# Optimization experiments

Hardware: AMD Instinct MI355X
Metric: run time of the kernel (lower is better)

## Reference

```python
import jax, jax.numpy as jnp
import numpy as np

N = 100000   # num visited nodes
D = 128      # emb_dim
B = 1024     # num queries (eg_idx groups)
DEG = 256    # edges per query group (fixed, > K so topk always prunes)
E = B * DEG  # 262144 edges
K = 20       # max_attended_edges
RATIO = 0.0  # ratio_update
NEG_SLOPE = 0.01  # LeakyReLU default


def segment_softmax(logits, seg, num_segments):
    m = jax.ops.segment_max(logits, seg, num_segments=num_segments)
    ex = jnp.exp(logits - m[seg])
    s = jax.ops.segment_sum(ex, seg, num_segments=num_segments)
    return ex / s[seg]


def setup_inputs() -> dict:
    key = jax.random.key(0)
    ks = jax.random.split(key, 11)
    node_score = jax.random.uniform(ks[0], (N,), dtype=jnp.float32)
    node_repr = jax.random.normal(ks[1], (N, D), dtype=jnp.float32)
    rel_emb = jax.random.normal(ks[2], (E, D), dtype=jnp.float32)
    q_src_emb = jax.random.normal(ks[3], (B, D), dtype=jnp.float32)
    q_rel_emb = jax.random.normal(ks[4], (B, D), dtype=jnp.float32)
    # G3: Linear(4D, 4D, bias=False), init normal std sqrt(2/dim_in)
    Wq = jax.random.normal(ks[5], (4 * D, 4 * D), dtype=jnp.float32) * np.sqrt(2.0 / (4 * D))
    Wk = jax.random.normal(ks[6], (4 * D, 4 * D), dtype=jnp.float32) * np.sqrt(2.0 / (4 * D))
    # linear_between_steps: Linear(D, D) xavier
    W_lin = jax.random.normal(ks[7], (D, D), dtype=jnp.float32) * np.sqrt(2.0 / (2 * D))
    b_lin = jnp.zeros((D,), dtype=jnp.float32)
    # edges: [E, 8]; col0 = eg_idx (sorted, fixed DEG per group), col6 = vi, col7 = vj
    eg = jnp.repeat(jnp.arange(B, dtype=jnp.int32), DEG)
    vi = jax.random.randint(ks[8], (E,), 0, N, dtype=jnp.int32)
    vj = jax.random.randint(ks[9], (E,), 0, N, dtype=jnp.int32)
    z = jnp.zeros((E,), dtype=jnp.int32)
    edges = jnp.stack([eg, z, z, z, z, z, vi, vj], axis=1)
    return {
        "node_score": node_score, "node_repr": node_repr, "rel_emb": rel_emb,
        "q_src_emb": q_src_emb, "q_rel_emb": q_rel_emb,
        "Wq": Wq, "Wk": Wk, "W_lin": W_lin, "b_lin": b_lin, "edges": edges,
    }


def reference(node_score, node_repr, rel_emb, q_src_emb, q_rel_emb, Wq, Wk, W_lin, b_lin, edges):
    eg = edges[:, 0]
    vi = edges[:, 6]
    vj = edges[:, 7]
    # --- G3 attention score over edges ---
    hvi = node_repr[vi]           # [E, D]
    hvj = node_repr[vj]           # [E, D]
    qst = q_src_emb[eg]           # [E, D]
    qr = q_rel_emb[eg]            # [E, D]
    left = jnp.concatenate([hvi, rel_emb, qst, qr], axis=-1)   # [E, 4D]
    right = jnp.concatenate([hvj, rel_emb, qst, qr], axis=-1)  # [E, 4D]
    logits = jnp.sum((left @ Wq.T) * (right @ Wk.T), axis=-1)  # [E]
    # --- segment softmax over source node vi ---
    sm = segment_softmax(logits, vi, N)
    src_score = node_score[vi]
    target_score = sm * src_score
    # --- per-query-group top-k edge pruning (fixed DEG per group) ---
    topk_vals, topk_idx = jax.lax.top_k(target_score.reshape(B, DEG), K)  # [B, K]
    flat_idx = (topk_idx + jnp.arange(B, dtype=topk_idx.dtype)[:, None] * DEG).reshape(-1)  # [B*K]
    p_vi = vi[flat_idx]
    p_vj = vj[flat_idx]
    p_sm = sm[flat_idx]
    p_src = src_score[flat_idx]
    # --- node score aggregation: scatter-sum sm*src_score into target node vj ---
    updated_node_score = jax.ops.segment_sum(p_sm * p_src, p_vj, num_segments=N)
    # --- node representation update (sparse transition + identity fill) ---
    agg = jax.ops.segment_sum((1.0 - RATIO) * p_sm[:, None] * node_repr[p_vj], p_vi, num_segments=N)
    appears = jnp.zeros((N,), dtype=jnp.float32).at[p_vi].set(1.0)
    self_coef = jnp.where(appears > 0, RATIO, 1.0)[:, None]
    updated_repr = agg + self_coef * node_repr
    # --- bypass_forward: LeakyReLU(Linear) ---
    updated_repr = jax.nn.leaky_relu(updated_repr @ W_lin.T + b_lin, NEG_SLOPE)
    return updated_node_score, updated_repr
```

## Files before the change

### kernel.cpp

```cpp
#include <hip/hip_runtime.h>

#define NN 100000
#define BQ 1024
#define EE 262144
#define KTOP 20

typedef unsigned long long ull;
typedef __attribute__((ext_vector_type(8))) short bf16x8;
typedef __attribute__((ext_vector_type(4))) float f32x4;

__device__ __forceinline__ ull enc64(double d) {
  ull u = (ull)__double_as_longlong(d);
  return (u >> 63) ? ~u : (u | 0x8000000000000000ull);
}
__device__ __forceinline__ double dec64(ull u) {
  ull b = (u >> 63) ? (u & 0x7FFFFFFFFFFFFFFFull) : ~u;
  return __longlong_as_double((long long)b);
}

__device__ __forceinline__ unsigned short f2bf(float f) {
  unsigned u = __float_as_uint(f);
  u += 0x7fff + ((u >> 16) & 1);
  return (unsigned short)(u >> 16);
}
__device__ __forceinline__ float bf2f(unsigned short h) {
  return __uint_as_float(((unsigned)h) << 16);
}
__device__ __forceinline__ void cvt8(float4 x, float4 y, bf16x8& hi, bf16x8& lo) {
  float a[8] = {x.x, x.y, x.z, x.w, y.x, y.y, y.z, y.w};
#pragma unroll
  for (int j = 0; j < 8; j++) {
    unsigned short h = f2bf(a[j]);
    float r = a[j] - bf2f(h);
    hi[j] = (short)h;
    lo[j] = (short)f2bf(r);
  }
}

__global__ void k_prep(const int* __restrict__ edges, int4* __restrict__ evi,
                       int* __restrict__ vi32, ull* __restrict__ menc,
                       double* __restrict__ s, float* __restrict__ appears,
                       float* __restrict__ out_score) {
  int i = blockIdx.x * 256 + threadIdx.x;
  int st = gridDim.x * 256;
  for (int e = i; e < EE; e += st) {
    int vi = edges[(size_t)e * 8 + 6];
    evi[e] = make_int4(edges[(size_t)e * 8 + 0], vi, edges[(size_t)e * 8 + 7], 0);
    vi32[e] = vi;
  }
  for (int n = i; n < NN; n += st) {
    menc[n] = 0ull;
    s[n] = 0.0;
    appears[n] = 0.f;
    out_score[n] = 0.f;
  }
}

__global__ void k_matM(const float* __restrict__ Wq, const float* __restrict__ Wk,
                       float* __restrict__ M, float* __restrict__ MT) {
  int x = blockIdx.x;
  int y = blockIdx.y * 256 + threadIdx.x;
  float acc = 0.f;
  for (int a = 0; a < 512; a++)
    acc += Wq[a * 512 + x] * Wk[a * 512 + y];
  M[x * 512 + y] = acc;
  MT[y * 512 + x] = acc;
}

__global__ void k_pack(const float* __restrict__ M, const float* __restrict__ MT,
                       const float* __restrict__ Wl,
                       short* __restrict__ wn_hi, short* __restrict__ wn_lo,
                       short* __restrict__ m11_hi, short* __restrict__ m11_lo,
                       short* __restrict__ wl_hi, short* __restrict__ wl_lo) {
  int idx = blockIdx.x * 256 + threadIdx.x;
  if (idx >= 5 * 16384) return;
  int arr = idx >> 14;
  int j16 = idx & 16383;
  int g = j16 >> 9;
  int l = (j16 >> 3) & 63;
  int jj = j16 & 7;
  int c = (g >> 2) * 16 + (l & 15);
  int k = (g & 3) * 32 + ((l >> 4) << 3) + jj;
  float v;
  short *dh, *dl;
  if (arr == 0)      { v = MT[(size_t)c * 512 + k];               dh = wn_hi;          dl = wn_lo; }
  else if (arr == 1) { v = MT[(size_t)(128 + c) * 512 + k];       dh = wn_hi + 16384;  dl = wn_lo + 16384; }
  else if (arr == 2) { v = M[(size_t)(128 + c) * 512 + k];        dh = wn_hi + 32768;  dl = wn_lo + 32768; }
  else if (arr == 3) { v = MT[(size_t)(128 + c) * 512 + 128 + k]; dh = m11_hi;         dl = m11_lo; }
  else               { v = Wl[(size_t)c * 128 + k];               dh = wl_hi;          dl = wl_lo; }
  unsigned short h = f2bf(v);
  float r = v - bf2f(h);
  dh[j16] = (short)h;
  dl[j16] = (short)f2bf(r);
}

__global__ void k_pq(const float* __restrict__ M, const float* __restrict__ MT,
                     const float* __restrict__ qsA, const float* __restrict__ qrA,
                     float* __restrict__ Qv, double* __restrict__ cq) {
  int b = blockIdx.x, d = threadIdx.x;
  __shared__ float qs[128], qr[128];
  qs[d] = qsA[b * 128 + d];
  qr[d] = qrA[b * 128 + d];
  __syncthreads();
  float uh = 0, ui = 0, ur = 0;
  for (int x = 0; x < 128; x++) {
    float qsx = qs[x], qrx = qr[x];
    uh += qsx * M[(256 + x) * 512 + d]        + qrx * M[(384 + x) * 512 + d];
    ur += qsx * M[(256 + x) * 512 + 128 + d]  + qrx * M[(384 + x) * 512 + 128 + d];
    ui += qsx * MT[(256 + x) * 512 + d]       + qrx * MT[(384 + x) * 512 + d];
    ur += qsx * MT[(256 + x) * 512 + 128 + d] + qrx * MT[(384 + x) * 512 + 128 + d];
  }
  Qv[b * 384 + d]       = uh;
  Qv[b * 384 + 128 + d] = ui;
  Qv[b * 384 + 256 + d] = ur;
  float t1 = 0, t2 = 0;
  for (int y = 0; y < 128; y++) {
    float qsy = qs[y], qry = qr[y];
    t1 += qsy * MT[(256 + y) * 512 + 256 + d] + qry * MT[(384 + y) * 512 + 256 + d];
    t2 += qsy * MT[(256 + y) * 512 + 384 + d] + qry * MT[(384 + y) * 512 + 384 + d];
  }
  float cp = qs[d] * t1 + qr[d] * t2;
  for (int off = 32; off; off >>= 1) cp += __shfl_down(cp, off, 64);
  __shared__ float red[2];
  if ((d & 63) == 0) red[d >> 6] = cp;
  __syncthreads();
  if (d == 0) cq[b] = (double)(red[0] + red[1]);
}

__global__ __launch_bounds__(512) void k_gemm_node(const float* __restrict__ A,
                                                   const short* __restrict__ WT_hi,
                                                   const short* __restrict__ WT_lo,
                                                   float* __restrict__ G,
                                                   float* __restrict__ H1,
                                                   float* __restrict__ J) {
  __shared__ __align__(16) float As[64][132];
  __shared__ __align__(16) short Bh[16384];
  float* Of = (float*)Bh;
  int t = threadIdx.x;
  int row0 = blockIdx.x * 64;
  int w = t >> 6, l = t & 63;
  int rt = w & 3;
  int c0 = (w >> 2) * 4;
#pragma unroll
  for (int i = 0; i < 4; i++) {
    int fi = t + i * 512;
    int r = fi >> 5, c4 = (fi & 31) * 4;
    float4 v = make_float4(0.f, 0.f, 0.f, 0.f);
    if (row0 + r < NN) v = *(const float4*)(A + (size_t)(row0 + r) * 128 + c4);
    *(float4*)&As[r][c4] = v;
    *(bf16x8*)&Bh[fi * 8] = *(const bf16x8*)(WT_hi + fi * 8);
  }
  __syncthreads();
  int rloc = rt * 16 + (l & 15);
  int kq = (l >> 4) * 8;
  for (int panel = 0; panel < 3; panel++) {
    const short* sl = WT_lo + panel * 16384;
    bf16x8 blv[4][4];
#pragma unroll
    for (int cc = 0; cc < 4; cc++)
#pragma unroll
      for (int kt = 0; kt < 4; kt++)
        blv[cc][kt] = *(const bf16x8*)(sl + (((c0 + cc) * 4 + kt) * 64 + l) * 8);
    f32x4 acc[4];
#pragma unroll
    for (int cc = 0; cc < 4; cc++)
#pragma unroll
      for (int j = 0; j < 4; j++) acc[cc][j] = 0.f;
#pragma unroll
    for (int kt = 0; kt < 4; kt++) {
      int kb = kt * 32 + kq;
      float4 x = *(const float4*)&As[rloc][kb];
      float4 y = *(const float4*)&As[rloc][kb + 4];
      bf16x8 ah, al;
      cvt8(x, y, ah, al);
#pragma unroll
      for (int cc = 0; cc < 4; cc++) {
        int off = (((cc + c0) * 4 + kt) * 64 + l) * 8;
        bf16x8 bhv = *(const bf16x8*)&Bh[off];
        acc[cc] = __builtin_amdgcn_mfma_f32_16x16x32_bf16(ah, bhv, acc[cc], 0, 0, 0);
        acc[cc] = __builtin_amdgcn_mfma_f32_16x16x32_bf16(al, bhv, acc[cc], 0, 0, 0);
        acc[cc] = __builtin_amdgcn_mfma_f32_16x16x32_bf16(ah, blv[cc][kt], acc[cc], 0, 0, 0);
      }
    }
    __syncthreads();
#pragma unroll
    for (int cc = 0; cc < 4; cc++) {
      int col = (c0 + cc) * 16 + (l & 15);
#pragma unroll
      for (int reg = 0; reg < 4; reg++)
        Of[(rt * 16 + (l >> 4) * 4 + reg) * 128 + col] = acc[cc][reg];
    }
    __syncthreads();
    float* dst = (panel == 0) ? G : (panel == 1) ? H1 : J;
#pragma unroll
    for (int i = 0; i < 4; i++) {
      int fi = t + i * 512;
      int r = fi >> 5, c4 = (fi & 31) * 4;
      int rr = row0 + r;
      if (rr < NN) *(float4*)&dst[(size_t)rr * 128 + c4] = *(float4*)&Of[r * 128 + c4];
    }
    if (panel < 2) {
      __syncthreads();
      const short* sh = WT_hi + (panel + 1) * 16384;
#pragma unroll
      for (int i = 0; i < 4; i++) {
        int fi = t + i * 512;
        *(bf16x8*)&Bh[fi * 8] = *(const bf16x8*)(sh + fi * 8);
      }
      __syncthreads();
    }
  }
}

__global__ __launch_bounds__(512, 1) void k_edge(const float* __restrict__ rel,
                                                 const short* __restrict__ M11T_hi,
                                                 const short* __restrict__ M11T_lo,
                                                 const int4* __restrict__ evi,
                                                 const float* __restrict__ H1,
                                                 const float* __restrict__ J,
                                                 const float* __restrict__ Qv,
                                                 float* __restrict__ rq) {
  __shared__ __align__(16) float Rs[64][132];
  __shared__ __align__(16) short Bh[16384];
  __shared__ float part[4][64];
  __shared__ float dg[64];
  __shared__ float urs[128];
  int t = threadIdx.x;
  int e0 = blockIdx.x * 64;
  int eg = e0 >> 8;
  int w = t >> 6, l = t & 63;
  int cq2 = w & 3;
  int rh = w >> 2;
  int gg = t >> 4, ll = t & 15, d = ll * 8;
  int4 edA = evi[e0 + gg * 2];
  int4 edB = evi[e0 + gg * 2 + 1];
  const float* pA1 = H1 + (size_t)edA.y * 128 + d;
  const float* pA2 = J + (size_t)edA.z * 128 + d;
  const float* pB1 = H1 + (size_t)edB.y * 128 + d;
  const float* pB2 = J + (size_t)edB.z * 128 + d;
  float4 Aa0 = *(const float4*)pA1, Aa1 = *(const float4*)(pA1 + 4);
  float4 Ab0 = *(const float4*)pA2, Ab1 = *(const float4*)(pA2 + 4);
  float4 Ba0 = *(const float4*)pB1, Ba1 = *(const float4*)(pB1 + 4);
  float4 Bb0 = *(const float4*)pB2, Bb1 = *(const float4*)(pB2 + 4);
  bf16x8 blv[2][4];
#pragma unroll
  for (int cc = 0; cc < 2; cc++)
#pragma unroll
    for (int kt = 0; kt < 4; kt++)
      blv[cc][kt] = *(const bf16x8*)(M11T_lo + (((cq2 * 2 + cc) * 4 + kt) * 64 + l) * 8);
#pragma unroll
  for (int i = 0; i < 4; i++) {
    int fi = t + i * 512;
    int r = fi >> 5, c4 = (fi & 31) * 4;
    *(float4*)&Rs[r][c4] = *(const float4*)(rel + (size_t)(e0 + r) * 128 + c4);
    *(bf16x8*)&Bh[fi * 8] = *(const bf16x8*)(M11T_hi + fi * 8);
  }
  if (t < 128) urs[t] = Qv[(size_t)eg * 384 + 256 + t];
  __syncthreads();
  int kq = (l >> 4) * 8;
  int rq4 = (l >> 4) * 4;
#pragma unroll
  for (int rt2 = 0; rt2 < 2; rt2++) {
    int rt = rh * 2 + rt2;
    int rloc = rt * 16 + (l & 15);
    f32x4 acc[2];
#pragma unroll
    for (int cc = 0; cc < 2; cc++)
#pragma unroll
      for (int j = 0; j < 4; j++) acc[cc][j] = 0.f;
#pragma unroll
    for (int kt = 0; kt < 4; kt++) {
      int kb = kt * 32 + kq;
      float4 x = *(const float4*)&Rs[rloc][kb];
      float4 y = *(const float4*)&Rs[rloc][kb + 4];
      bf16x8 ah, al;
      cvt8(x, y, ah, al);
#pragma unroll
      for (int cc = 0; cc < 2; cc++) {
        bf16x8 bhv = *(const bf16x8*)&Bh[(((cq2 * 2 + cc) * 4 + kt) * 64 + l) * 8];
        acc[cc] = __builtin_amdgcn_mfma_f32_16x16x32_bf16(ah, bhv, acc[cc], 0, 0, 0);
        acc[cc] = __builtin_amdgcn_mfma_f32_16x16x32_bf16(al, bhv, acc[cc], 0, 0, 0);
        acc[cc] = __builtin_amdgcn_mfma_f32_16x16x32_bf16(ah, blv[cc][kt], acc[cc], 0, 0, 0);
      }
    }
    float p[4] = {0.f, 0.f, 0.f, 0.f};
#pragma unroll
    for (int cc = 0; cc < 2; cc++) {
      int c = (cq2 * 2 + cc) * 16 + (l & 15);
#pragma unroll
      for (int reg = 0; reg < 4; reg++)
        p[reg] += acc[cc][reg] * Rs[rt * 16 + rq4 + reg][c];
    }
#pragma unroll
    for (int reg = 0; reg < 4; reg++) {
      p[reg] += __shfl_xor(p[reg], 1, 64);
      p[reg] += __shfl_xor(p[reg], 2, 64);
      p[reg] += __shfl_xor(p[reg], 4, 64);
      p[reg] += __shfl_xor(p[reg], 8, 64);
    }
    if ((l & 15) == 0) {
#pragma unroll
      for (int reg = 0; reg < 4; reg++) part[cq2][rt * 16 + rq4 + reg] = p[reg];
    }
  }
  float4 u0 = *(const float4*)&urs[d], u1 = *(const float4*)&urs[d + 4];
  {
    int le = gg * 2;
    float4 r0 = *(const float4*)&Rs[le][d], r1 = *(const float4*)&Rs[le][d + 4];
    float dot = (Aa0.x + Ab0.x + u0.x) * r0.x + (Aa0.y + Ab0.y + u0.y) * r0.y
              + (Aa0.z + Ab0.z + u0.z) * r0.z + (Aa0.w + Ab0.w + u0.w) * r0.w
              + (Aa1.x + Ab1.x + u1.x) * r1.x + (Aa1.y + Ab1.y + u1.y) * r1.y
              + (Aa1.z + Ab1.z + u1.z) * r1.z + (Aa1.w + Ab1.w + u1.w) * r1.w;
    dot += __shfl_xor(dot, 1, 64);
    dot += __shfl_xor(dot, 2, 64);
    dot += __shfl_xor(dot, 4, 64);
    dot += __shfl_xor(dot, 8, 64);
    if (ll == 0) dg[le] = dot;
  }
  {
    int le = gg * 2 + 1;
    float4 r0 = *(const float4*)&Rs[le][d], r1 = *(const float4*)&Rs[le][d + 4];
    float dot = (Ba0.x + Bb0.x + u0.x) * r0.x + (Ba0.y + Bb0.y + u0.y) * r0.y
              + (Ba0.z + Bb0.z + u0.z) * r0.z + (Ba0.w + Bb0.w + u0.w) * r0.w
              + (Ba1.x + Bb1.x + u1.x) * r1.x + (Ba1.y + Bb1.y + u1.y) * r1.y
              + (Ba1.z + Bb1.z + u1.z) * r1.z + (Ba1.w + Bb1.w + u1.w) * r1.w;
    dot += __shfl_xor(dot, 1, 64);
    dot += __shfl_xor(dot, 2, 64);
    dot += __shfl_xor(dot, 4, 64);
    dot += __shfl_xor(dot, 8, 64);
    if (ll == 0) dg[le] = dot;
  }
  __syncthreads();
  if (t < 64)
    rq[e0 + t] = ((part[0][t] + part[1][t]) + (part[2][t] + part[3][t])) + dg[t];
}

__global__ __launch_bounds__(256) void k_logits(const int4* __restrict__ evi,
                                                const float* __restrict__ nrep,
                                                const float* __restrict__ G,
                                                const float* __restrict__ Qv,
                                                const double* __restrict__ cq,
                                                const float* __restrict__ rq,
                                                double* __restrict__ logits,
                                                ull* __restrict__ menc) {
  int t = threadIdx.x;
  int ll = t & 15;
  int grp = (t & 63) >> 4;
  int wid = blockIdx.x * 4 + (t >> 6);
  int nw = gridDim.x * 4;
  int d = ll * 8;
  for (int e4 = wid; e4 < EE / 4; e4 += nw) {
    int e = e4 * 4 + grp;
    int4 ed = evi[e];
    int eg = ed.x, vi = ed.y, vj = ed.z;
    const float* gp = G + (size_t)vi * 128 + d;
    const float* hi = nrep + (size_t)vi * 128 + d;
    const float* hj = nrep + (size_t)vj * 128 + d;
    const float* q  = Qv + (size_t)eg * 384 + d;
    float4 g0  = *(const float4*)gp,        g1  = *(const float4*)(gp + 4);
    float4 a0  = *(const float4*)hi,        a1  = *(const float4*)(hi + 4);
    float4 b0  = *(const float4*)hj,        b1  = *(const float4*)(hj + 4);
    float4 uh0 = *(const float4*)q,         uh1 = *(const float4*)(q + 4);
    float4 ui0 = *(const float4*)(q + 128), ui1 = *(const float4*)(q + 132);
    float acc;
    acc  = (g0.x + uh0.x) * b0.x + (g0.y + uh0.y) * b0.y
         + (g0.z + uh0.z) * b0.z + (g0.w + uh0.w) * b0.w
         + (g1.x + uh1.x) * b1.x + (g1.y + uh1.y) * b1.y
         + (g1.z + uh1.z) * b1.z + (g1.w + uh1.w) * b1.w;
    acc += ui0.x * a0.x + ui0.y * a0.y + ui0.z * a0.z + ui0.w * a0.w
         + ui1.x * a1.x + ui1.y * a1.y + ui1.z * a1.z + ui1.w * a1.w;
    acc += __shfl_xor(acc, 1, 64);
    acc += __shfl_xor(acc, 2, 64);
    acc += __shfl_xor(acc, 4, 64);
    acc += __shfl_xor(acc, 8, 64);
    if (ll == 0) {
      double l2 = (double)acc + cq[eg] + (double)rq[e];
      logits[e] = l2;
      atomicMax(&menc[vi], enc64(l2));
    }
  }
}

__global__ void k_exp(const int* __restrict__ vi32, const ull* __restrict__ menc,
                      const double* __restrict__ logits, double* __restrict__ ex,
                      double* __restrict__ s, float4* __restrict__ agg) {
  int i = blockIdx.x * 256 + threadIdx.x;
  int st = gridDim.x * 256;
  for (int e = i; e < EE; e += st) {
    int vi = vi32[e];
    double m = dec64(menc[vi]);
    double v = exp(logits[e] - m);
    ex[e] = v;
    atomicAdd(&s[vi], v);
  }
  const int n4 = NN * 32;
  for (int n = i; n < n4; n += st) agg[n] = make_float4(0.f, 0.f, 0.f, 0.f);
}

__global__ void k_topk(const double* __restrict__ ex, const double* __restrict__ s,
                       const float* __restrict__ nscore, const int4* __restrict__ evi,
                       const float* __restrict__ nrep, float* __restrict__ out_score,
                       float* __restrict__ agg, float* __restrict__ appears) {
  int b = blockIdx.x, t = threadIdx.x;
  int e = b * 256 + t;
  int vi_t = evi[e].y;
  double v = ex[e] / s[vi_t] * (double)nscore[vi_t];
  __shared__ double cv[80];
  __shared__ int ci[80];
  __shared__ int winners[KTOP];
  int w = t >> 6;
  for (int k = 0; k < KTOP; k++) {
    double bv = v;
    int bi = t;
    for (int off = 32; off; off >>= 1) {
      double ov = __shfl_down(bv, off, 64);
      int oi = __shfl_down(bi, off, 64);
      if (ov > bv || (ov == bv && oi < bi)) { bv = ov; bi = oi; }
    }
    bi = __shfl(bi, 0, 64);
    if ((t & 63) == 0) { cv[w * KTOP + k] = bv; ci[w * KTOP + k] = bi; }
    if (t == bi) v = -1.0;
  }
  __syncthreads();
  if (t < 64) {
    double v0 = cv[t];
    int i0 = ci[t];
    double v1 = (t < 16) ? cv[64 + t] : -2.0;
    int i1 = (t < 16) ? ci[64 + t] : (1 << 30);
    for (int k = 0; k < KTOP; k++) {
      double bv; int bi;
      if (v1 > v0 || (v1 == v0 && i1 < i0)) { bv = v1; bi = i1; }
      else                                  { bv = v0; bi = i0; }
      for (int off = 32; off; off >>= 1) {
        double ov = __shfl_down(bv, off, 64);
        int oi = __shfl_down(bi, off, 64);
        if (ov > bv || (ov == bv && oi < bi)) { bv = ov; bi = oi; }
      }
      bi = __shfl(bi, 0, 64);
      if (t == 0) winners[k] = bi;
      if (i0 == bi) v0 = -2.0;
      if (i1 == bi) v1 = -2.0;
    }
  }
  __syncthreads();
  for (int k = 0; k < KTOP; k++) {
    int we = b * 256 + winners[k];
    int4 ew = evi[we];
    int vi = ew.y, vj = ew.z;
    double sm = ex[we] / s[vi];
    if (t < 128) {
      atomicAdd(&agg[(size_t)vi * 128 + t], (float)sm * nrep[(size_t)vj * 128 + t]);
    } else if (t == 128) {
      atomicAdd(&out_score[vj], (float)(sm * (double)nscore[vi]));
    } else if (t == 129) {
      appears[vi] = 1.f;
    }
  }
}

__global__ __launch_bounds__(512) void k_final(const float* __restrict__ agg,
                                               const float* __restrict__ appears,
                                               const float* __restrict__ nrep,
                                               const short* __restrict__ Wl_hi,
                                               const short* __restrict__ Wl_lo,
                                               const float* __restrict__ bl,
                                               float* __restrict__ outr) {
  __shared__ __align__(16) float Xs[64][132];
  __shared__ __align__(16) short Bh[16384];
  int t = threadIdx.x;
  int row0 = blockIdx.x * 64;
  int w = t >> 6, l = t & 63;
  int rt = w & 3;
  int c0 = (w >> 2) * 4;
  bf16x8 blv[4][4];
#pragma unroll
  for (int cc = 0; cc < 4; cc++)
#pragma unroll
    for (int kt = 0; kt < 4; kt++)
      blv[cc][kt] = *(const bf16x8*)(Wl_lo + (((c0 + cc) * 4 + kt) * 64 + l) * 8);
#pragma unroll
  for (int i = 0; i < 4; i++) {
    int fi = t + i * 512;
    int r = fi >> 5, c4 = (fi & 31) * 4;
    int rr = row0 + r;
    float4 v = make_float4(0.f, 0.f, 0.f, 0.f);
    if (rr < NN) {
      float4 ag = *(const float4*)(agg + (size_t)rr * 128 + c4);
      float4 h = *(const float4*)(nrep + (size_t)rr * 128 + c4);
      float coef = (appears[rr] > 0.f) ? 0.f : 1.f;
      v.x = ag.x + coef * h.x;
      v.y = ag.y + coef * h.y;
      v.z = ag.z + coef * h.z;
      v.w = ag.w + coef * h.w;
    }
    *(float4*)&Xs[r][c4] = v;
    *(bf16x8*)&Bh[fi * 8] = *(const bf16x8*)(Wl_hi + fi * 8);
  }
  __syncthreads();
  int rloc = rt * 16 + (l & 15);
  int kq = (l >> 4) * 8;
  f32x4 acc[4];
#pragma unroll
  for (int cc = 0; cc < 4; cc++)
#pragma unroll
    for (int j = 0; j < 4; j++) acc[cc][j] = 0.f;
#pragma unroll
  for (int kt = 0; kt < 4; kt++) {
    int kb = kt * 32 + kq;
    float4 x = *(const float4*)&Xs[rloc][kb];
    float4 y = *(const float4*)&Xs[rloc][kb + 4];
    bf16x8 ah, al;
    cvt8(x, y, ah, al);
#pragma unroll
    for (int cc = 0; cc < 4; cc++) {
      int off = (((c0 + cc) * 4 + kt) * 64 + l) * 8;
      bf16x8 bhv = *(const bf16x8*)&Bh[off];
      acc[cc] = __builtin_amdgcn_mfma_f32_16x16x32_bf16(ah, bhv, acc[cc], 0, 0, 0);
      acc[cc] = __builtin_amdgcn_mfma_f32_16x16x32_bf16(al, bhv, acc[cc], 0, 0, 0);
      acc[cc] = __builtin_amdgcn_mfma_f32_16x16x32_bf16(ah, blv[cc][kt], acc[cc], 0, 0, 0);
    }
  }
  __syncthreads();
#pragma unroll
  for (int cc = 0; cc < 4; cc++) {
    int col = (c0 + cc) * 16 + (l & 15);
#pragma unroll
    for (int reg = 0; reg < 4; reg++)
      Xs[rt * 16 + (l >> 4) * 4 + reg][col] = acc[cc][reg];
  }
  __syncthreads();
#pragma unroll
  for (int i = 0; i < 4; i++) {
    int fi = t + i * 512;
    int r = fi >> 5, c4 = (fi & 31) * 4;
    int rr = row0 + r;
    if (rr < NN) {
      float4 v = *(float4*)&Xs[r][c4];
      float4 bb = *(const float4*)&bl[c4];
      float4 o;
      o.x = v.x + bb.x; o.x = (o.x > 0.f) ? o.x : 0.01f * o.x;
      o.y = v.y + bb.y; o.y = (o.y > 0.f) ? o.y : 0.01f * o.y;
      o.z = v.z + bb.z; o.z = (o.z > 0.f) ? o.z : 0.01f * o.z;
      o.w = v.w + bb.w; o.w = (o.w > 0.f) ? o.w : 0.01f * o.w;
      *(float4*)&outr[(size_t)rr * 128 + c4] = o;
    }
  }
}

extern "C" void kernel_launch(void* const* d_in, const int* in_sizes, int n_in,
                              void* d_out, int out_size, void* d_ws, size_t ws_size,
                              hipStream_t stream) {
  const float* node_score = (const float*)d_in[0];
  const float* node_repr  = (const float*)d_in[1];
  const float* rel_emb    = (const float*)d_in[2];
  const float* q_src      = (const float*)d_in[3];
  const float* q_rel      = (const float*)d_in[4];
  const float* Wq         = (const float*)d_in[5];
  const float* Wk         = (const float*)d_in[6];
  const float* W_lin      = (const float*)d_in[7];
  const float* b_lin      = (const float*)d_in[8];
  const int*   edges      = (const int*)d_in[9];

  char* ws = (char*)d_ws;
  size_t off = 0;
  auto carve = [&](size_t bytes) -> void* {
    void* p = ws + off;
    off += (bytes + 255) & ~(size_t)255;
    return p;
  };
  float*  M      = (float*)carve(512 * 512 * 4);
  float*  MT     = (float*)carve(512 * 512 * 4);
  short*  wn_hi  = (short*)carve(3 * 16384 * 2);
  short*  wn_lo  = (short*)carve(3 * 16384 * 2);
  short*  m11_hi = (short*)carve(16384 * 2);
  short*  m11_lo = (short*)carve(16384 * 2);
  short*  wl_hi  = (short*)carve(16384 * 2);
  short*  wl_lo  = (short*)carve(16384 * 2);
  float*  Qv     = (float*)carve((size_t)BQ * 384 * 4);
  double* cq     = (double*)carve((size_t)BQ * 8);
  double* logits = (double*)carve((size_t)EE * 8);
  float*  rq     = (float*)carve((size_t)EE * 4);
  ull*    menc   = (ull*)carve((size_t)NN * 8);
  double* s      = (double*)carve((size_t)NN * 8);
  double* ex     = (double*)carve((size_t)EE * 8);
  float*  appears= (float*)carve((size_t)NN * 4);
  int4*   evi    = (int4*)carve((size_t)EE * 16);
  int*    vi32   = (int*)carve((size_t)EE * 4);
  float*  G      = (float*)carve((size_t)NN * 128 * 4);
  float*  H1     = (float*)carve((size_t)NN * 128 * 4);
  float*  J      = (float*)carve((size_t)NN * 128 * 4);
  float*  agg    = G;

  float* out_score = (float*)d_out;
  float* out_repr  = (float*)d_out + NN;

  k_prep<<<1024, 256, 0, stream>>>(edges, evi, vi32, menc, s, appears, out_score);
  k_matM<<<dim3(512, 2), 256, 0, stream>>>(Wq, Wk, M, MT);
  k_pack<<<320, 256, 0, stream>>>(M, MT, W_lin, wn_hi, wn_lo, m11_hi, m11_lo, wl_hi, wl_lo);
  k_pq<<<BQ, 128, 0, stream>>>(M, MT, q_src, q_rel, Qv, cq);
  k_gemm_node<<<1563, 512, 0, stream>>>(node_repr, wn_hi, wn_lo, G, H1, J);
  k_edge<<<4096, 512, 0, stream>>>(rel_emb, m11_hi, m11_lo, evi, H1, J, Qv, rq);
  k_logits<<<8192, 256, 0, stream>>>(evi, node_repr, G, Qv, cq, rq, logits, menc);
  k_exp<<<2048, 256, 0, stream>>>(vi32, menc, logits, ex, s, (float4*)agg);
  k_topk<<<BQ, 256, 0, stream>>>(ex, s, node_score, evi, node_repr, out_score, agg, appears);
  k_final<<<1563, 512, 0, stream>>>(agg, appears, node_repr, wl_hi, wl_lo, b_lin, out_repr);
}
```

Before: 380.6 us.

## Fuse logits computation and segment-max atomics into the edge kernel

Merges the separate k_logits kernel into k_edge, so each block computes the gathered G/node_repr dot products for its 64 edges, adds the rel-based partials and cq, and writes logits and atomicMax directly. This removes the rq intermediate buffer round-trip, one kernel launch, and the re-reads of evi and Qv. The gather loads are issued before the final barrier to overlap with the matrix work. The cost is more register pressure in a block already launched with 512 threads at one block per CU, and a different parallel mapping for the gather phase.

Result: faster. 369.1 us, median of 2 (-3.0%).

```diff
diff --git a/kernel.cpp b/kernel.cpp
--- a/kernel.cpp
+++ b/kernel.cpp
@@ -218,13 +218,18 @@
                                                  const int4* __restrict__ evi,
                                                  const float* __restrict__ H1,
                                                  const float* __restrict__ J,
+                                                 const float* __restrict__ G,
+                                                 const float* __restrict__ nrep,
                                                  const float* __restrict__ Qv,
-                                                 float* __restrict__ rq) {
+                                                 const double* __restrict__ cq,
+                                                 double* __restrict__ logits,
+                                                 ull* __restrict__ menc) {
   __shared__ __align__(16) float Rs[64][132];
   __shared__ __align__(16) short Bh[16384];
   __shared__ float part[4][64];
   __shared__ float dg[64];
-  __shared__ float urs[128];
+  __shared__ float uhs[128], uis[128], urs[128];
+  __shared__ double cqs;
   int t = threadIdx.x;
   int e0 = blockIdx.x * 64;
   int eg = e0 >> 8;
@@ -255,7 +260,12 @@
     *(float4*)&Rs[r][c4] = *(const float4*)(rel + (size_t)(e0 + r) * 128 + c4);
     *(bf16x8*)&Bh[fi * 8] = *(const bf16x8*)(M11T_hi + fi * 8);
   }
-  if (t < 128) urs[t] = Qv[(size_t)eg * 384 + 256 + t];
+  if (t < 128) {
+    uhs[t] = Qv[(size_t)eg * 384 + t];
+    uis[t] = Qv[(size_t)eg * 384 + 128 + t];
+    urs[t] = Qv[(size_t)eg * 384 + 256 + t];
+  }
+  if (t == 0) cqs = cq[eg];
   __syncthreads();
   int kq = (l >> 4) * 8;
   int rq4 = (l >> 4) * 4;
@@ -330,53 +340,57 @@
     dot += __shfl_xor(dot, 8, 64);
     if (ll == 0) dg[le] = dot;
   }
-  __syncthreads();
-  if (t < 64)
-    rq[e0 + t] = ((part[0][t] + part[1][t]) + (part[2][t] + part[3][t])) + dg[t];
-}
-
-__global__ __launch_bounds__(256) void k_logits(const int4* __restrict__ evi,
-                                                const float* __restrict__ nrep,
-                                                const float* __restrict__ G,
-                                                const float* __restrict__ Qv,
-                                                const double* __restrict__ cq,
-                                                const float* __restrict__ rq,
-                                                double* __restrict__ logits,
-                                                ull* __restrict__ menc) {
-  int t = threadIdx.x;
-  int ll = t & 15;
-  int grp = (t & 63) >> 4;
-  int wid = blockIdx.x * 4 + (t >> 6);
-  int nw = gridDim.x * 4;
-  int d = ll * 8;
-  for (int e4 = wid; e4 < EE / 4; e4 += nw) {
-    int e = e4 * 4 + grp;
-    int4 ed = evi[e];
-    int eg = ed.x, vi = ed.y, vj = ed.z;
-    const float* gp = G + (size_t)vi * 128 + d;
-    const float* hi = nrep + (size_t)vi * 128 + d;
-    const float* hj = nrep + (size_t)vj * 128 + d;
-    const float* q  = Qv + (size_t)eg * 384 + d;
-    float4 g0  = *(const float4*)gp,        g1  = *(const float4*)(gp + 4);
-    float4 a0  = *(const float4*)hi,        a1  = *(const float4*)(hi + 4);
-    float4 b0  = *(const float4*)hj,        b1  = *(const float4*)(hj + 4);
-    float4 uh0 = *(const float4*)q,         uh1 = *(const float4*)(q + 4);
-    float4 ui0 = *(const float4*)(q + 128), ui1 = *(const float4*)(q + 132);
-    float acc;
-    acc  = (g0.x + uh0.x) * b0.x + (g0.y + uh0.y) * b0.y
-         + (g0.z + uh0.z) * b0.z + (g0.w + uh0.w) * b0.w
-         + (g1.x + uh1.x) * b1.x + (g1.y + uh1.y) * b1.y
-         + (g1.z + uh1.z) * b1.z + (g1.w + uh1.w) * b1.w;
-    acc += ui0.x * a0.x + ui0.y * a0.y + ui0.z * a0.z + ui0.w * a0.w
-         + ui1.x * a1.x + ui1.y * a1.y + ui1.z * a1.z + ui1.w * a1.w;
-    acc += __shfl_xor(acc, 1, 64);
-    acc += __shfl_xor(acc, 2, 64);
-    acc += __shfl_xor(acc, 4, 64);
-    acc += __shfl_xor(acc, 8, 64);
+  const float* gA  = G + (size_t)edA.y * 128 + d;
+  const float* iA  = nrep + (size_t)edA.y * 128 + d;
+  const float* jA  = nrep + (size_t)edA.z * 128 + d;
+  const float* gB  = G + (size_t)edB.y * 128 + d;
+  const float* iB  = nrep + (size_t)edB.y * 128 + d;
+  const float* jB  = nrep + (size_t)edB.z * 128 + d;
+  float4 GA0 = *(const float4*)gA, GA1 = *(const float4*)(gA + 4);
+  float4 IA0 = *(const float4*)iA, IA1 = *(const float4*)(iA + 4);
+  float4 JA0 = *(const float4*)jA, JA1 = *(const float4*)(jA + 4);
+  float4 GB0 = *(const float4*)gB, GB1 = *(const float4*)(gB + 4);
+  float4 IB0 = *(const float4*)iB, IB1 = *(const float4*)(iB + 4);
+  float4 JB0 = *(const float4*)jB, JB1 = *(const float4*)(jB + 4);
+  __syncthreads();
+  float4 h0 = *(const float4*)&uhs[d], h1 = *(const float4*)&uhs[d + 4];
+  float4 i0 = *(const float4*)&uis[d], i1 = *(const float4*)&uis[d + 4];
+  {
+    int le = gg * 2;
+    float gd = (GA0.x + h0.x) * JA0.x + (GA0.y + h0.y) * JA0.y
+             + (GA0.z + h0.z) * JA0.z + (GA0.w + h0.w) * JA0.w
+             + (GA1.x + h1.x) * JA1.x + (GA1.y + h1.y) * JA1.y
+             + (GA1.z + h1.z) * JA1.z + (GA1.w + h1.w) * JA1.w
+             + i0.x * IA0.x + i0.y * IA0.y + i0.z * IA0.z + i0.w * IA0.w
+             + i1.x * IA1.x + i1.y * IA1.y + i1.z * IA1.z + i1.w * IA1.w;
+    gd += __shfl_xor(gd, 1, 64);
+    gd += __shfl_xor(gd, 2, 64);
+    gd += __shfl_xor(gd, 4, 64);
+    gd += __shfl_xor(gd, 8, 64);
     if (ll == 0) {
-      double l2 = (double)acc + cq[eg] + (double)rq[e];
-      logits[e] = l2;
-      atomicMax(&menc[vi], enc64(l2));
+      float base = ((part[0][le] + part[1][le]) + (part[2][le] + part[3][le])) + dg[le] + gd;
+      double l2 = (double)base + cqs;
+      logits[e0 + le] = l2;
+      atomicMax(&menc[edA.y], enc64(l2));
+    }
+  }
+  {
+    int le = gg * 2 + 1;
+    float gd = (GB0.x + h0.x) * JB0.x + (GB0.y + h0.y) * JB0.y
+             + (GB0.z + h0.z) * JB0.z + (GB0.w + h0.w) * JB0.w
+             + (GB1.x + h1.x) * JB1.x + (GB1.y + h1.y) * JB1.y
+             + (GB1.z + h1.z) * JB1.z + (GB1.w + h1.w) * JB1.w
+             + i0.x * IB0.x + i0.y * IB0.y + i0.z * IB0.z + i0.w * IB0.w
+             + i1.x * IB1.x + i1.y * IB1.y + i1.z * IB1.z + i1.w * IB1.w;
+    gd += __shfl_xor(gd, 1, 64);
+    gd += __shfl_xor(gd, 2, 64);
+    gd += __shfl_xor(gd, 4, 64);
+    gd += __shfl_xor(gd, 8, 64);
+    if (ll == 0) {
+      float base = ((part[0][le] + part[1][le]) + (part[2][le] + part[3][le])) + dg[le] + gd;
+      double l2 = (double)base + cqs;
+      logits[e0 + le] = l2;
+      atomicMax(&menc[edB.y], enc64(l2));
     }
   }
 }
@@ -579,7 +593,6 @@
   float*  Qv     = (float*)carve((size_t)BQ * 384 * 4);
   double* cq     = (double*)carve((size_t)BQ * 8);
   double* logits = (double*)carve((size_t)EE * 8);
-  float*  rq     = (float*)carve((size_t)EE * 4);
   ull*    menc   = (ull*)carve((size_t)NN * 8);
   double* s      = (double*)carve((size_t)NN * 8);
   double* ex     = (double*)carve((size_t)EE * 8);
@@ -599,8 +612,7 @@
   k_pack<<<320, 256, 0, stream>>>(M, MT, W_lin, wn_hi, wn_lo, m11_hi, m11_lo, wl_hi, wl_lo);
   k_pq<<<BQ, 128, 0, stream>>>(M, MT, q_src, q_rel, Qv, cq);
   k_gemm_node<<<1563, 512, 0, stream>>>(node_repr, wn_hi, wn_lo, G, H1, J);
-  k_edge<<<4096, 512, 0, stream>>>(rel_emb, m11_hi, m11_lo, evi, H1, J, Qv, rq);
-  k_logits<<<8192, 256, 0, stream>>>(evi, node_repr, G, Qv, cq, rq, logits, menc);
+  k_edge<<<4096, 512, 0, stream>>>(rel_emb, m11_hi, m11_lo, evi, H1, J, G, node_repr, Qv, cq, logits, menc);
   k_exp<<<2048, 256, 0, stream>>>(vi32, menc, logits, ex, s, (float4*)agg);
   k_topk<<<BQ, 256, 0, stream>>>(ex, s, node_score, evi, node_repr, out_score, agg, appears);
   k_final<<<1563, 512, 0, stream>>>(agg, appears, node_repr, wl_hi, wl_lo, b_lin, out_repr);
```
